# Kernel tuning notes

Hardware: AMD Instinct MI355X
Metric: run time of the kernel (lower is better)

## Reference

```python
import jax, jax.numpy as jnp
import numpy as np

PATCH = 16      # sqrt(n_patches=256)
ALPHA = 10.0
HEADS, DH = 2, 64


def _fourier(coords, Bm):
    # coords: (HW, 2), Bm: (n_features, 2) -> (HW, 2*n_features)
    proj = 2.0 * jnp.pi * coords @ Bm.T
    return jnp.concatenate([jnp.cos(proj), jnp.sin(proj)], axis=-1)


def _forward(coords_decoding, tokens, B_q, B_l0, B_l1,
             qW, qb, toqW, tokvW, tooW, toob,
             bwW0, bwb0, bwW1, bwb1,
             modW0, modb0, modW1, modb1,
             hvW0, hvb0, outW0, outb0, outW1, outb1):
    B = coords_decoding.shape[0]
    Hh, Ww = coords_decoding.shape[1], coords_decoding.shape[2]
    coords = coords_decoding.reshape(B, -1, coords_decoding.shape[-1])
    grid = coords[0]                      # (HW, 2); coords_modulation is None -> same grid
    HW = grid.shape[0]
    m = tokens.shape[1]

    # patch indices and spatial bias
    row = jnp.clip((grid[:, 0] * PATCH).astype(jnp.int32), 0, PATCH - 1)
    col = jnp.clip((grid[:, 1] * PATCH).astype(jnp.int32), 0, PATCH - 1)
    idx = row * PATCH + col               # (HW,)
    t = idx.astype(jnp.float32) / (PATCH * PATCH)
    pos = (jnp.arange(m, dtype=jnp.float32) + 0.5) / m
    rel = -ALPHA * jnp.abs(t[None, :] - pos[:, None]) ** 2   # (m, HW)
    bias = rel.T                          # (HW, m), broadcast over batch & heads

    # query features (shared across batch)
    xq = jax.nn.relu(_fourier(grid, B_q) @ qW + qb)           # (HW, hd)
    xq_b = jnp.broadcast_to(xq[None], (B, HW, xq.shape[-1]))

    # cross attention with spatial bias
    q = (xq_b @ toqW).reshape(B, HW, HEADS, DH).transpose(0, 2, 1, 3)   # (B,h,HW,Dh)
    kv = tokens @ tokvW                                                  # (B,m,2*inner)
    k, v = jnp.split(kv, 2, axis=-1)
    k = k.reshape(B, m, HEADS, DH).transpose(0, 2, 1, 3)                 # (B,h,m,Dh)
    v = v.reshape(B, m, HEADS, DH).transpose(0, 2, 1, 3)
    sim = jnp.einsum('bhqd,bhkd->bhqk', q, k) * (DH ** -0.5) + bias[None, None]
    attn = jax.nn.softmax(sim, axis=-1)
    o = jnp.einsum('bhqk,bhkd->bhqd', attn, v)
    o = o.transpose(0, 2, 1, 3).reshape(B, HW, HEADS * DH)
    mod = o @ tooW + toob                                                # (B,HW,hd)

    # per-band MLP stack (layer_num = 2)
    def band(Bl, bwW, bwb, mW, mb):
        h = jax.nn.relu(_fourier(grid, Bl) @ bwW + bwb)                  # (HW,hd)
        return jax.nn.relu(h[None] + mod @ mW + mb)                      # (B,HW,hd)

    m0 = band(B_l0, bwW0, bwb0, modW0, modb0)
    m1 = band(B_l1, bwW1, bwb1, modW1, modb1)
    hv0 = m0
    hv1 = jax.nn.relu((m1 + hv0) @ hvW0 + hvb0)
    out = (hv0 @ outW0 + outb0) + (hv1 @ outW1 + outb1)                  # (B,HW,3)
    return out.reshape(B, Hh, Ww, -1)


def setup_inputs() -> dict:
    key = jax.random.key(0)
    ks = jax.random.split(key, 32)
    B, H, W, L = 4, 128, 128, 256
    fd, hd, cd, od = 64, 256, 256, 3
    nf = fd // 2
    inner = HEADS * DH

    def lin(k, i, o):
        return jax.random.normal(k, (i, o), dtype=jnp.float32) / np.sqrt(i).astype(np.float32)

    inp = {}
    inp['coords_decoding'] = jax.random.uniform(ks[0], (B, H, W, 2), dtype=jnp.float32)
    inp['tokens'] = jax.random.normal(ks[1], (B, L, cd), dtype=jnp.float32)
    inp['B_q'] = jax.random.normal(ks[2], (nf, 2), dtype=jnp.float32) / 16.0
    inp['B_l0'] = jax.random.normal(ks[3], (nf, 2), dtype=jnp.float32) / 128.0
    inp['B_l1'] = jax.random.normal(ks[4], (nf, 2), dtype=jnp.float32) / 32.0
    inp['qW'] = lin(ks[5], fd, hd); inp['qb'] = jnp.zeros((hd,), jnp.float32)
    inp['toqW'] = lin(ks[6], hd, inner)
    inp['tokvW'] = lin(ks[7], cd, inner * 2)
    inp['tooW'] = lin(ks[8], inner, hd); inp['toob'] = jnp.zeros((hd,), jnp.float32)
    inp['bwW0'] = lin(ks[9], fd, hd); inp['bwb0'] = jnp.zeros((hd,), jnp.float32)
    inp['bwW1'] = lin(ks[10], fd, hd); inp['bwb1'] = jnp.zeros((hd,), jnp.float32)
    inp['modW0'] = lin(ks[11], hd, hd); inp['modb0'] = jnp.zeros((hd,), jnp.float32)
    inp['modW1'] = lin(ks[12], hd, hd); inp['modb1'] = jnp.zeros((hd,), jnp.float32)
    inp['hvW0'] = lin(ks[13], hd, hd); inp['hvb0'] = jnp.zeros((hd,), jnp.float32)
    inp['outW0'] = lin(ks[14], hd, od); inp['outb0'] = jnp.zeros((od,), jnp.float32)
    inp['outW1'] = lin(ks[15], hd, od); inp['outb1'] = jnp.zeros((od,), jnp.float32)
    return inp


def reference(coords_decoding, tokens, B_q, B_l0, B_l1,
              qW, qb, toqW, tokvW, tooW, toob,
              bwW0, bwb0, bwW1, bwb1,
              modW0, modb0, modW1, modb1,
              hvW0, hvb0, outW0, outb0, outW1, outb1):
    return _forward(coords_decoding, tokens, B_q, B_l0, B_l1,
                    qW, qb, toqW, tokvW, tooW, toob,
                    bwW0, bwb0, bwW1, bwb1,
                    modW0, modb0, modW1, modb1,
                    hvW0, hvb0, outW0, outb0, outW1, outb1)
```

## Files before the change

### kernel.cpp

```cpp
#include <hip/hip_runtime.h>
#include <stdint.h>

constexpr int kHW = 16384;
constexpr int kB  = 4;
constexpr int kM  = 256;

typedef _Float16 half8 __attribute__((ext_vector_type(8)));
typedef __attribute__((ext_vector_type(4))) float f32x4;

__device__ __forceinline__ unsigned short f2h(float f) {
  _Float16 h = (_Float16)f;
  return __builtin_bit_cast(unsigned short, h);
}
__device__ __forceinline__ float h2f(unsigned short u) {
  return (float)__builtin_bit_cast(_Float16, u);
}

__global__ __launch_bounds__(256) void wprep_kernel(
    const float* __restrict__ tooW, const float* __restrict__ modW0,
    const float* __restrict__ modW1, const float* __restrict__ hvW0,
    const float* __restrict__ qW, const float* __restrict__ bwW0,
    const float* __restrict__ bwW1, const float* __restrict__ toqW,
    unsigned short* __restrict__ tooWt, unsigned short* __restrict__ modW0t,
    unsigned short* __restrict__ modW1t, unsigned short* __restrict__ hvW0t,
    unsigned short* __restrict__ qWt, unsigned short* __restrict__ bw0t,
    unsigned short* __restrict__ bw1t, unsigned short* __restrict__ toqWt)
{
  int m = blockIdx.x, tid = threadIdx.x;
  const float* Ws[8] = {tooW, modW0, modW1, hvW0, qW, bwW0, bwW1, toqW};
  unsigned short* Wts[8] = {tooWt, modW0t, modW1t, hvW0t, qWt, bw0t, bw1t, toqWt};
  const int Ks[8] = {128, 256, 256, 256, 64, 64, 64, 256};
  const int Ns[8] = {256, 256, 256, 256, 256, 256, 256, 128};
  const float* W = Ws[m];
  unsigned short* Wt = Wts[m];
  int K = Ks[m], N = Ns[m];
  if (tid < N) {
    for (int kb = 0; kb < K / 8; kb++) {
      unsigned short sv[8];
#pragma unroll
      for (int i = 0; i < 8; i++)
        sv[i] = f2h(W[(kb * 8 + i) * N + tid]);
      *(uint4*)&Wt[tid * K + kb * 8] = *(const uint4*)sv;
    }
  }
}

__global__ __launch_bounds__(256) void kv_kernel(
    const float* __restrict__ tokens, const float* __restrict__ tokvW,
    unsigned short* __restrict__ kn_ws, unsigned short* __restrict__ vt_ws)
{
  __shared__ __align__(16) float tok[256];
  int b = blockIdx.y, j = blockIdx.x, c = threadIdx.x;
  tok[c] = tokens[(b * kM + j) * 256 + c];
  __syncthreads();
  float acc = 0.f;
  for (int i4 = 0; i4 < 64; i4++) {
    float4 t4 = *(const float4*)&tok[i4 * 4];
    acc += t4.x * tokvW[(i4*4+0)*256 + c] + t4.y * tokvW[(i4*4+1)*256 + c]
         + t4.z * tokvW[(i4*4+2)*256 + c] + t4.w * tokvW[(i4*4+3)*256 + c];
  }
  unsigned short hv = f2h(acc);
  if (c < 128) {
    int h = c >> 6, dd = c & 63;
    kn_ws[((size_t)(b*2+h)*256 + j) * 64 + dd] = hv;
  } else {
    int c2 = c - 128;
    int h = c2 >> 6, dd = c2 & 63;
    vt_ws[((size_t)(b*2+h)*64 + dd) * 256 + j] = hv;
  }
}

constexpr int kFPitch = 72;
constexpr int kXPitch = 264;

__global__ __launch_bounds__(256, 2) void feat_kernel(
    const float* __restrict__ coords,
    const float* __restrict__ Bq, const float* __restrict__ Bl0, const float* __restrict__ Bl1,
    const float* __restrict__ qb, const float* __restrict__ bwb0, const float* __restrict__ bwb1,
    const unsigned short* __restrict__ qWt, const unsigned short* __restrict__ bw0t,
    const unsigned short* __restrict__ bw1t, const unsigned short* __restrict__ toqWt,
    float* __restrict__ t_ws, unsigned short* __restrict__ qc_ws,
    unsigned short* __restrict__ h0_hf, unsigned short* __restrict__ h1_hf)
{
  __shared__ __align__(16) unsigned short ff_s[3][32][kFPitch];
  __shared__ __align__(16) unsigned short xq_s[32][kXPitch];
  __shared__ float coords_s[64];

  int tid = threadIdx.x;
  int px0 = blockIdx.x * 32;
  int w = tid >> 6, ln = tid & 63;
  int c = ln & 15, q = ln >> 4;

  if (tid < 64) coords_s[tid] = coords[px0 * 2 + tid];
  __syncthreads();

#pragma unroll
  for (int r = 0; r < 24; r++) {
    int v = r * 256 + tid;
    int mat = v >> 11;
    int p = (v >> 6) & 31;
    int f = v & 63;
    int fr = f & 31;
    const float* Bm = (mat == 0) ? Bq : (mat == 1 ? Bl0 : Bl1);
    float x = coords_s[p * 2 + 0];
    float y = coords_s[p * 2 + 1];
    float proj = 6.283185307179586f * (x * Bm[fr*2+0] + y * Bm[fr*2+1]);
    float s, cc;
    __sincosf(proj, &s, &cc);
    ff_s[mat][p][f] = f2h((f < 32) ? cc : s);
  }
  if (tid < 32) {
    float x = coords_s[tid * 2 + 0];
    float y = coords_s[tid * 2 + 1];
    int row = min(max((int)(x * 16.0f), 0), 15);
    int col = min(max((int)(y * 16.0f), 0), 15);
    t_ws[px0 + tid] = (float)(row * 16 + col) * (1.0f / 256.0f);
  }
  __syncthreads();

  const f32x4 zero4 = {0.f, 0.f, 0.f, 0.f};

  for (int mat = 0; mat < 3; mat++) {
    const unsigned short* Wt = (mat == 0) ? qWt : (mat == 1 ? bw0t : bw1t);
    const float* bias = (mat == 0) ? qb : (mat == 1 ? bwb0 : bwb1);
    f32x4 acc[8];
#pragma unroll
    for (int i = 0; i < 8; i++) acc[i] = zero4;
#pragma unroll
    for (int ks = 0; ks < 2; ks++) {
      int koff = ks * 32 + q * 8;
      half8 bfr[4];
#pragma unroll
      for (int nt = 0; nt < 4; nt++)
        bfr[nt] = *(const half8*)(Wt + (size_t)(w*64 + nt*16 + c) * 64 + koff);
      half8 afr[2];
#pragma unroll
      for (int mt = 0; mt < 2; mt++)
        afr[mt] = *(const half8*)(&ff_s[mat][mt*16 + c][koff]);
#pragma unroll
      for (int mt = 0; mt < 2; mt++)
#pragma unroll
        for (int nt = 0; nt < 4; nt++)
          acc[mt*4+nt] = __builtin_amdgcn_mfma_f32_16x16x32_f16(afr[mt], bfr[nt], acc[mt*4+nt], 0, 0, 0);
    }
    float bv[4];
#pragma unroll
    for (int nt = 0; nt < 4; nt++) bv[nt] = bias[w*64 + nt*16 + c];
#pragma unroll
    for (int mt = 0; mt < 2; mt++)
#pragma unroll
      for (int nt = 0; nt < 4; nt++)
#pragma unroll
        for (int rg = 0; rg < 4; rg++) {
          int row = mt*16 + q*4 + rg, col = w*64 + nt*16 + c;
          unsigned short hv = f2h(fmaxf(acc[mt*4+nt][rg] + bv[nt], 0.f));
          if (mat == 0)      xq_s[row][col] = hv;
          else if (mat == 1) h0_hf[((size_t)(px0 + row)) * 256 + col] = hv;
          else               h1_hf[((size_t)(px0 + row)) * 256 + col] = hv;
        }
  }
  __syncthreads();

  {
    f32x4 acc2[4];
#pragma unroll
    for (int i = 0; i < 4; i++) acc2[i] = zero4;
#pragma unroll
    for (int kt = 0; kt < 8; kt++) {
      int koff = kt * 32 + q * 8;
      half8 bfr[2];
#pragma unroll
      for (int nt = 0; nt < 2; nt++)
        bfr[nt] = *(const half8*)(toqWt + (size_t)(w*32 + nt*16 + c) * 256 + koff);
      half8 afr[2];
#pragma unroll
      for (int mt = 0; mt < 2; mt++)
        afr[mt] = *(const half8*)(&xq_s[mt*16 + c][koff]);
#pragma unroll
      for (int mt = 0; mt < 2; mt++)
#pragma unroll
        for (int nt = 0; nt < 2; nt++)
          acc2[mt*2+nt] = __builtin_amdgcn_mfma_f32_16x16x32_f16(afr[mt], bfr[nt], acc2[mt*2+nt], 0, 0, 0);
    }
#pragma unroll
    for (int mt = 0; mt < 2; mt++)
#pragma unroll
      for (int nt = 0; nt < 2; nt++)
#pragma unroll
        for (int rg = 0; rg < 4; rg++) {
          int row = mt*16 + q*4 + rg, col = w*32 + nt*16 + c;
          qc_ws[((size_t)(px0 + row)) * 128 + col] = f2h(acc2[mt*2+nt][rg]);
        }
  }
}

constexpr int kPPitch = 264;

__global__ __launch_bounds__(256, 2) void attn_kernel(
    const unsigned short* __restrict__ kn_ws,
    const unsigned short* __restrict__ vt_ws,
    const unsigned short* __restrict__ qc_ws,
    const float* __restrict__ t_ws,
    unsigned short* __restrict__ o_hf)
{
  __shared__ __align__(16) unsigned short P_s[32 * kPPitch];
  __shared__ float t_s[32];
  __shared__ float red_max[32][4];
  __shared__ float red_sum[32][4];

  int b = blockIdx.y;
  int px0 = blockIdx.x * 32;
  int tid = threadIdx.x;
  int w = tid >> 6, ln = tid & 63;
  int c = ln & 15, q = ln >> 4;

  if (tid < 32) t_s[tid] = t_ws[px0 + tid];

  const f32x4 zero4 = {0.f, 0.f, 0.f, 0.f};

  for (int h = 0; h < 2; h++) {
    __syncthreads();

    f32x4 acc[8];
#pragma unroll
    for (int i = 0; i < 8; i++) acc[i] = zero4;
    const unsigned short* kbase = kn_ws + (size_t)(b*2+h) * 256 * 64;
#pragma unroll
    for (int ks = 0; ks < 2; ks++) {
      int koff = ks * 32 + q * 8;
      half8 a0 = *(const half8*)(qc_ws + (size_t)(px0 + c) * 128 + h*64 + koff);
      half8 a1 = *(const half8*)(qc_ws + (size_t)(px0 + 16 + c) * 128 + h*64 + koff);
#pragma unroll
      for (int nt = 0; nt < 4; nt++) {
        half8 bf = *(const half8*)(kbase + (size_t)(w*64 + nt*16 + c) * 64 + koff);
        acc[0*4+nt] = __builtin_amdgcn_mfma_f32_16x16x32_f16(a0, bf, acc[0*4+nt], 0, 0, 0);
        acc[1*4+nt] = __builtin_amdgcn_mfma_f32_16x16x32_f16(a1, bf, acc[1*4+nt], 0, 0, 0);
      }
    }

    float lm[2][4];
#pragma unroll
    for (int mt = 0; mt < 2; mt++)
#pragma unroll
      for (int rg = 0; rg < 4; rg++) {
        int row = mt*16 + q*4 + rg;
        float tv = t_s[row];
        float mx = -1e30f;
#pragma unroll
        for (int nt = 0; nt < 4; nt++) {
          int token = w*64 + nt*16 + c;
          float pos = ((float)token + 0.5f) * (1.0f / 256.0f);
          float db = tv - pos;
          float sb = acc[mt*4+nt][rg] * 0.125f - 10.0f * db * db;
          acc[mt*4+nt][rg] = sb;
          mx = fmaxf(mx, sb);
        }
        lm[mt][rg] = mx;
      }
#pragma unroll
    for (int s = 1; s < 16; s <<= 1)
#pragma unroll
      for (int mt = 0; mt < 2; mt++)
#pragma unroll
        for (int rg = 0; rg < 4; rg++)
          lm[mt][rg] = fmaxf(lm[mt][rg], __shfl_xor(lm[mt][rg], s, 64));
    if (c == 0) {
#pragma unroll
      for (int mt = 0; mt < 2; mt++)
#pragma unroll
        for (int rg = 0; rg < 4; rg++)
          red_max[mt*16 + q*4 + rg][w] = lm[mt][rg];
    }
    __syncthreads();

    float ps[2][4];
#pragma unroll
    for (int mt = 0; mt < 2; mt++)
#pragma unroll
      for (int rg = 0; rg < 4; rg++) {
        int row = mt*16 + q*4 + rg;
        float gm = fmaxf(fmaxf(red_max[row][0], red_max[row][1]),
                         fmaxf(red_max[row][2], red_max[row][3]));
        float sum = 0.f;
#pragma unroll
        for (int nt = 0; nt < 4; nt++) {
          float e = __expf(acc[mt*4+nt][rg] - gm);
          sum += e;
          P_s[row * kPPitch + w*64 + nt*16 + c] = f2h(e);
        }
        ps[mt][rg] = sum;
      }
#pragma unroll
    for (int s = 1; s < 16; s <<= 1)
#pragma unroll
      for (int mt = 0; mt < 2; mt++)
#pragma unroll
        for (int rg = 0; rg < 4; rg++)
          ps[mt][rg] += __shfl_xor(ps[mt][rg], s, 64);
    if (c == 0) {
#pragma unroll
      for (int mt = 0; mt < 2; mt++)
#pragma unroll
        for (int rg = 0; rg < 4; rg++)
          red_sum[mt*16 + q*4 + rg][w] = ps[mt][rg];
    }
    __syncthreads();

    f32x4 oacc[2] = {zero4, zero4};
    const unsigned short* vbase = vt_ws + (size_t)(b*2+h) * 64 * 256;
#pragma unroll
    for (int kt = 0; kt < 8; kt++) {
      int koff = kt * 32 + q * 8;
      half8 bf = *(const half8*)(vbase + (size_t)(w*16 + c) * 256 + koff);
      half8 a0 = *(const half8*)(P_s + (0*16 + c) * kPPitch + koff);
      half8 a1 = *(const half8*)(P_s + (1*16 + c) * kPPitch + koff);
      oacc[0] = __builtin_amdgcn_mfma_f32_16x16x32_f16(a0, bf, oacc[0], 0, 0, 0);
      oacc[1] = __builtin_amdgcn_mfma_f32_16x16x32_f16(a1, bf, oacc[1], 0, 0, 0);
    }
#pragma unroll
    for (int mt = 0; mt < 2; mt++)
#pragma unroll
      for (int rg = 0; rg < 4; rg++) {
        int row = mt*16 + q*4 + rg;
        float rinv = 1.0f / (red_sum[row][0] + red_sum[row][1] +
                             red_sum[row][2] + red_sum[row][3]);
        o_hf[((size_t)(b * kHW + px0 + row)) * 128 + h*64 + w*16 + c] =
            f2h(oacc[mt][rg] * rinv);
      }
  }
}

constexpr int kPitch = 264;

template <int KD>
__device__ __forceinline__ void gemm4(
    const unsigned short* abuf, const unsigned short* wt,
    f32x4* acc , int c, int q)
{
#pragma unroll
  for (int ks = 0; ks < KD / 32; ks++) {
    int koff = ks * 32 + q * 8;
    half8 bfr[4];
#pragma unroll
    for (int nt = 0; nt < 4; nt++)
      bfr[nt] = *(const half8*)(wt + (nt * 16 + c) * KD + koff);
    half8 afr[4];
#pragma unroll
    for (int mt = 0; mt < 4; mt++)
      afr[mt] = *(const half8*)(abuf + (mt * 16 + c) * kPitch + koff);
#pragma unroll
    for (int mt = 0; mt < 4; mt++)
#pragma unroll
      for (int nt = 0; nt < 4; nt++)
        acc[mt * 4 + nt] = __builtin_amdgcn_mfma_f32_16x16x32_f16(afr[mt], bfr[nt], acc[mt * 4 + nt], 0, 0, 0);
  }
}

__global__ __launch_bounds__(256, 2) void mlp_kernel(
    const unsigned short* __restrict__ o_hf,
    const unsigned short* __restrict__ h0_hf, const unsigned short* __restrict__ h1_hf,
    const unsigned short* __restrict__ tooWt, const float* __restrict__ toob,
    const unsigned short* __restrict__ modW0t, const float* __restrict__ modb0,
    const unsigned short* __restrict__ modW1t, const float* __restrict__ modb1,
    const unsigned short* __restrict__ hvW0t, const float* __restrict__ hvb0,
    const float* __restrict__ outW0, const float* __restrict__ outb0,
    const float* __restrict__ outW1, const float* __restrict__ outb1,
    float* __restrict__ dout)
{
  __shared__ __align__(16) unsigned short buf0[64 * kPitch];
  __shared__ __align__(16) unsigned short buf1[64 * kPitch];
  __shared__ __align__(16) unsigned short hbuf[16 * kPitch];
  __shared__ __align__(16) float scratch[64 * 3 * 4];

  int tid = threadIdx.x;
  int px0 = blockIdx.x * 16;
  int w = tid >> 6, ln = tid & 63;
  int c = ln & 15, q = ln >> 4;

#pragma unroll
  for (int i = 0; i < 4; i++) {
    int idx = i * 256 + tid;
    int r = idx >> 4, c8 = (idx & 15) * 8;
    int b = r >> 4, px = r & 15;
    uint4 v = *(const uint4*)(o_hf + ((size_t)(b * kHW + px0 + px)) * 128 + c8);
    *(uint4*)&buf0[r * kPitch + c8] = v;
  }
#pragma unroll
  for (int i = 0; i < 2; i++) {
    int idx = i * 256 + tid;
    int p = idx >> 5, c8 = (idx & 31) * 8;
    uint4 v = *(const uint4*)(h0_hf + ((size_t)(px0 + p)) * 256 + c8);
    *(uint4*)&hbuf[p * kPitch + c8] = v;
  }
  __syncthreads();

  f32x4 acc[16];
  const f32x4 zero4 = {0.f, 0.f, 0.f, 0.f};

#pragma unroll
  for (int i = 0; i < 16; i++) acc[i] = zero4;
  gemm4<128>(buf0, tooWt + (size_t)w * 64 * 128, acc, c, q);
  {
    float bias[4];
#pragma unroll
    for (int nt = 0; nt < 4; nt++) bias[nt] = toob[w * 64 + nt * 16 + c];
#pragma unroll
    for (int mt = 0; mt < 4; mt++)
#pragma unroll
      for (int nt = 0; nt < 4; nt++)
#pragma unroll
        for (int rg = 0; rg < 4; rg++) {
          int row = mt * 16 + q * 4 + rg, col = w * 64 + nt * 16 + c;
          buf1[row * kPitch + col] = f2h(acc[mt * 4 + nt][rg] + bias[nt]);
        }
  }
  __syncthreads();

#pragma unroll
  for (int i = 0; i < 16; i++) acc[i] = zero4;
  gemm4<256>(buf1, modW0t + (size_t)w * 64 * 256, acc, c, q);
  {
    float bias[4], hr[4][4];
#pragma unroll
    for (int nt = 0; nt < 4; nt++) {
      int col = w * 64 + nt * 16 + c;
      bias[nt] = modb0[col];
#pragma unroll
      for (int rg = 0; rg < 4; rg++)
        hr[nt][rg] = h2f(hbuf[(q * 4 + rg) * kPitch + col]);
    }
#pragma unroll
    for (int mt = 0; mt < 4; mt++)
#pragma unroll
      for (int nt = 0; nt < 4; nt++)
#pragma unroll
        for (int rg = 0; rg < 4; rg++) {
          int row = mt * 16 + q * 4 + rg, col = w * 64 + nt * 16 + c;
          buf0[row * kPitch + col] =
              f2h(fmaxf(acc[mt * 4 + nt][rg] + bias[nt] + hr[nt][rg], 0.f));
        }
  }
  __syncthreads();

#pragma unroll
  for (int i = 0; i < 2; i++) {
    int idx = i * 256 + tid;
    int p = idx >> 5, c8 = (idx & 31) * 8;
    uint4 v = *(const uint4*)(h1_hf + ((size_t)(px0 + p)) * 256 + c8);
    *(uint4*)&hbuf[p * kPitch + c8] = v;
  }
#pragma unroll
  for (int i = 0; i < 16; i++) acc[i] = zero4;
  gemm4<256>(buf1, modW1t + (size_t)w * 64 * 256, acc, c, q);
  __syncthreads();
  {
    float bias[4], hr[4][4];
#pragma unroll
    for (int nt = 0; nt < 4; nt++) {
      int col = w * 64 + nt * 16 + c;
      bias[nt] = modb1[col];
#pragma unroll
      for (int rg = 0; rg < 4; rg++)
        hr[nt][rg] = h2f(hbuf[(q * 4 + rg) * kPitch + col]);
    }
#pragma unroll
    for (int mt = 0; mt < 4; mt++)
#pragma unroll
      for (int nt = 0; nt < 4; nt++)
#pragma unroll
        for (int rg = 0; rg < 4; rg++) {
          int row = mt * 16 + q * 4 + rg, col = w * 64 + nt * 16 + c;
          float m0v = h2f(buf0[row * kPitch + col]);
          float v = m0v + fmaxf(acc[mt * 4 + nt][rg] + bias[nt] + hr[nt][rg], 0.f);
          buf1[row * kPitch + col] = f2h(v);
        }
  }
  __syncthreads();

#pragma unroll
  for (int i = 0; i < 16; i++) acc[i] = zero4;
  gemm4<256>(buf1, hvW0t + (size_t)w * 64 * 256, acc, c, q);
  {
    float bias[4], w0v[4][3], w1v[4][3];
#pragma unroll
    for (int nt = 0; nt < 4; nt++) {
      int col = w * 64 + nt * 16 + c;
      bias[nt] = hvb0[col];
#pragma unroll
      for (int k = 0; k < 3; k++) {
        w0v[nt][k] = outW0[col * 3 + k];
        w1v[nt][k] = outW1[col * 3 + k];
      }
    }
#pragma unroll
    for (int mt = 0; mt < 4; mt++) {
      float pk[4][3];
#pragma unroll
      for (int rg = 0; rg < 4; rg++)
#pragma unroll
        for (int k = 0; k < 3; k++) pk[rg][k] = 0.f;
#pragma unroll
      for (int nt = 0; nt < 4; nt++) {
        int col = w * 64 + nt * 16 + c;
#pragma unroll
        for (int rg = 0; rg < 4; rg++) {
          int row = mt * 16 + q * 4 + rg;
          float hv1 = fmaxf(acc[mt * 4 + nt][rg] + bias[nt], 0.f);
          float m0v = h2f(buf0[row * kPitch + col]);
#pragma unroll
          for (int k = 0; k < 3; k++)
            pk[rg][k] += m0v * w0v[nt][k] + hv1 * w1v[nt][k];
        }
      }
#pragma unroll
      for (int s = 1; s < 16; s <<= 1)
#pragma unroll
        for (int rg = 0; rg < 4; rg++)
#pragma unroll
          for (int k = 0; k < 3; k++)
            pk[rg][k] += __shfl_xor(pk[rg][k], s, 64);
      if (c == 0) {
#pragma unroll
        for (int rg = 0; rg < 4; rg++) {
          int row = mt * 16 + q * 4 + rg;
#pragma unroll
          for (int k = 0; k < 3; k++)
            scratch[row * 12 + k * 4 + w] = pk[rg][k];
        }
      }
    }
  }
  __syncthreads();

  if (tid < 192) {
    int row = tid / 3, k = tid % 3;
    int b = row >> 4, px = px0 + (row & 15);
    float s = outb0[k] + outb1[k];
#pragma unroll
    for (int ww = 0; ww < 4; ww++) s += scratch[row * 12 + k * 4 + ww];
    dout[((size_t)b * kHW + px) * 3 + k] = s;
  }
}

extern "C" void kernel_launch(void* const* d_in, const int* in_sizes, int n_in,
                              void* d_out, int out_size, void* d_ws, size_t ws_size,
                              hipStream_t stream) {
  const float* coords = (const float*)d_in[0];
  const float* tokens = (const float*)d_in[1];
  const float* Bq     = (const float*)d_in[2];
  const float* Bl0    = (const float*)d_in[3];
  const float* Bl1    = (const float*)d_in[4];
  const float* qW     = (const float*)d_in[5];
  const float* qb     = (const float*)d_in[6];
  const float* toqW   = (const float*)d_in[7];
  const float* tokvW  = (const float*)d_in[8];
  const float* tooW   = (const float*)d_in[9];
  const float* toob   = (const float*)d_in[10];
  const float* bwW0   = (const float*)d_in[11];
  const float* bwb0   = (const float*)d_in[12];
  const float* bwW1   = (const float*)d_in[13];
  const float* bwb1   = (const float*)d_in[14];
  const float* modW0  = (const float*)d_in[15];
  const float* modb0  = (const float*)d_in[16];
  const float* modW1  = (const float*)d_in[17];
  const float* modb1  = (const float*)d_in[18];
  const float* hvW0   = (const float*)d_in[19];
  const float* hvb0   = (const float*)d_in[20];
  const float* outW0  = (const float*)d_in[21];
  const float* outb0  = (const float*)d_in[22];
  const float* outW1  = (const float*)d_in[23];
  const float* outb1  = (const float*)d_in[24];

  char* ws = (char*)d_ws;
  float*          t_ws   = (float*)(ws + 0);
  unsigned short* qc_ws  = (unsigned short*)(ws + 65536);
  unsigned short* h0_hf  = (unsigned short*)(ws + 4259840);
  unsigned short* h1_hf  = (unsigned short*)(ws + 12648448);
  unsigned short* o_hf   = (unsigned short*)(ws + 21037056);
  unsigned short* kn_ws  = (unsigned short*)(ws + 37814272);
  unsigned short* vt_ws  = (unsigned short*)(ws + 38076416);
  unsigned short* tooWt  = (unsigned short*)(ws + 38338560);
  unsigned short* modW0t = (unsigned short*)(ws + 38404096);
  unsigned short* modW1t = (unsigned short*)(ws + 38535168);
  unsigned short* hvW0t  = (unsigned short*)(ws + 38666240);
  unsigned short* qWt    = (unsigned short*)(ws + 38797312);
  unsigned short* bw0t   = (unsigned short*)(ws + 38830080);
  unsigned short* bw1t   = (unsigned short*)(ws + 38862848);
  unsigned short* toqWt  = (unsigned short*)(ws + 38895616);

  wprep_kernel<<<dim3(8), 256, 0, stream>>>(
      tooW, modW0, modW1, hvW0, qW, bwW0, bwW1, toqW,
      tooWt, modW0t, modW1t, hvW0t, qWt, bw0t, bw1t, toqWt);
  feat_kernel<<<dim3(kHW / 32), 256, 0, stream>>>(
      coords, Bq, Bl0, Bl1, qb, bwb0, bwb1,
      qWt, bw0t, bw1t, toqWt,
      t_ws, qc_ws, h0_hf, h1_hf);
  kv_kernel<<<dim3(kM, kB), 256, 0, stream>>>(tokens, tokvW, kn_ws, vt_ws);
  attn_kernel<<<dim3(kHW / 32, kB), 256, 0, stream>>>(kn_ws, vt_ws, qc_ws, t_ws, o_hf);
  mlp_kernel<<<dim3(kHW / 16), 256, 0, stream>>>(
      o_hf, h0_hf, h1_hf, tooWt, toob, modW0t, modb0, modW1t, modb1,
      hvW0t, hvb0, outW0, outb0, outW1, outb1, (float*)d_out);
}
```

Baseline: 257.3 us.

## Swizzle LDS buffers and keep m0 in registers to shrink MLP shared memory

Replaces the padded LDS pitches with XOR-swizzled layouts in both the attention P buffer and the MLP activation buffers. The MLP kernel now keeps the m0 activation packed as fp16 pairs in registers, so the second 64x256 LDS buffer is no longer needed. It also loads h0 and h1 together up front and raises the launch bound to three blocks per SM. The aim is to avoid bank conflicts and cut LDS use so more blocks fit per CU. The cost is 32 extra live registers per thread, which may cause spilling or work against the higher occupancy target.

Result: slower. 365.4 us (+42.0%).

```diff
diff --git a/kernel.cpp b/kernel.cpp
--- a/kernel.cpp
+++ b/kernel.cpp
@@ -14,6 +14,19 @@
 }
 __device__ __forceinline__ float h2f(unsigned short u) {
   return (float)__builtin_bit_cast(_Float16, u);
+}
+__device__ __forceinline__ float unpk(unsigned p, int hi) {
+  return h2f((unsigned short)(p >> (hi * 16)));
+}
+__device__ __forceinline__ int swz256(int row, int col) {
+  int ch = col >> 3;
+  ch = (ch & ~7) | ((ch ^ row) & 7);
+  return row * 256 + ch * 8 + (col & 7);
+}
+__device__ __forceinline__ int swz128(int row, int col) {
+  int ch = col >> 3;
+  ch = (ch & 8) | ((ch ^ row) & 7);
+  return row * 128 + ch * 8 + (col & 7);
 }
 
 __global__ __launch_bounds__(256) void wprep_kernel(
@@ -194,8 +207,6 @@
   }
 }
 
-constexpr int kPPitch = 264;
-
 __global__ __launch_bounds__(256, 2) void attn_kernel(
     const unsigned short* __restrict__ kn_ws,
     const unsigned short* __restrict__ vt_ws,
@@ -203,7 +214,7 @@
     const float* __restrict__ t_ws,
     unsigned short* __restrict__ o_hf)
 {
-  __shared__ __align__(16) unsigned short P_s[32 * kPPitch];
+  __shared__ __align__(16) unsigned short P_s[32 * 256];
   __shared__ float t_s[32];
   __shared__ float red_max[32][4];
   __shared__ float red_sum[32][4];
@@ -286,7 +297,7 @@
         for (int nt = 0; nt < 4; nt++) {
           float e = __expf(acc[mt*4+nt][rg] - gm);
           sum += e;
-          P_s[row * kPPitch + w*64 + nt*16 + c] = f2h(e);
+          P_s[swz256(row, w*64 + nt*16 + c)] = f2h(e);
         }
         ps[mt][rg] = sum;
       }
@@ -312,8 +323,8 @@
     for (int kt = 0; kt < 8; kt++) {
       int koff = kt * 32 + q * 8;
       half8 bf = *(const half8*)(vbase + (size_t)(w*16 + c) * 256 + koff);
-      half8 a0 = *(const half8*)(P_s + (0*16 + c) * kPPitch + koff);
-      half8 a1 = *(const half8*)(P_s + (1*16 + c) * kPPitch + koff);
+      half8 a0 = *(const half8*)(&P_s[swz256(c, koff)]);
+      half8 a1 = *(const half8*)(&P_s[swz256(16 + c, koff)]);
       oacc[0] = __builtin_amdgcn_mfma_f32_16x16x32_f16(a0, bf, oacc[0], 0, 0, 0);
       oacc[1] = __builtin_amdgcn_mfma_f32_16x16x32_f16(a1, bf, oacc[1], 0, 0, 0);
     }
@@ -330,33 +341,7 @@
   }
 }
 
-constexpr int kPitch = 264;
-
-template <int KD>
-__device__ __forceinline__ void gemm4(
-    const unsigned short* abuf, const unsigned short* wt,
-    f32x4* acc , int c, int q)
-{
-#pragma unroll
-  for (int ks = 0; ks < KD / 32; ks++) {
-    int koff = ks * 32 + q * 8;
-    half8 bfr[4];
-#pragma unroll
-    for (int nt = 0; nt < 4; nt++)
-      bfr[nt] = *(const half8*)(wt + (nt * 16 + c) * KD + koff);
-    half8 afr[4];
-#pragma unroll
-    for (int mt = 0; mt < 4; mt++)
-      afr[mt] = *(const half8*)(abuf + (mt * 16 + c) * kPitch + koff);
-#pragma unroll
-    for (int mt = 0; mt < 4; mt++)
-#pragma unroll
-      for (int nt = 0; nt < 4; nt++)
-        acc[mt * 4 + nt] = __builtin_amdgcn_mfma_f32_16x16x32_f16(afr[mt], bfr[nt], acc[mt * 4 + nt], 0, 0, 0);
-  }
-}
-
-__global__ __launch_bounds__(256, 2) void mlp_kernel(
+__global__ __launch_bounds__(256, 3) void mlp_kernel(
     const unsigned short* __restrict__ o_hf,
     const unsigned short* __restrict__ h0_hf, const unsigned short* __restrict__ h1_hf,
     const unsigned short* __restrict__ tooWt, const float* __restrict__ toob,
@@ -367,9 +352,8 @@
     const float* __restrict__ outW1, const float* __restrict__ outb1,
     float* __restrict__ dout)
 {
-  __shared__ __align__(16) unsigned short buf0[64 * kPitch];
-  __shared__ __align__(16) unsigned short buf1[64 * kPitch];
-  __shared__ __align__(16) unsigned short hbuf[16 * kPitch];
+  __shared__ __align__(16) unsigned short abuf[64 * 256];
+  __shared__ __align__(16) unsigned short obuf[8448];
   __shared__ __align__(16) float scratch[64 * 3 * 4];
 
   int tid = threadIdx.x;
@@ -377,109 +361,165 @@
   int w = tid >> 6, ln = tid & 63;
   int c = ln & 15, q = ln >> 4;
 
+  const f32x4 zero4 = {0.f, 0.f, 0.f, 0.f};
+  f32x4 acc[16];
+
 #pragma unroll
   for (int i = 0; i < 4; i++) {
     int idx = i * 256 + tid;
-    int r = idx >> 4, c8 = (idx & 15) * 8;
+    int r = idx >> 4, ch = idx & 15;
     int b = r >> 4, px = r & 15;
-    uint4 v = *(const uint4*)(o_hf + ((size_t)(b * kHW + px0 + px)) * 128 + c8);
-    *(uint4*)&buf0[r * kPitch + c8] = v;
+    uint4 v = *(const uint4*)(o_hf + ((size_t)(b * kHW + px0 + px)) * 128 + ch * 8);
+    *(uint4*)&obuf[swz128(r, ch * 8)] = v;
+  }
+  __syncthreads();
+
+#pragma unroll
+  for (int i = 0; i < 16; i++) acc[i] = zero4;
+#pragma unroll
+  for (int ks = 0; ks < 4; ks++) {
+    int koff = ks * 32 + q * 8;
+    half8 bfr[4];
+#pragma unroll
+    for (int nt = 0; nt < 4; nt++)
+      bfr[nt] = *(const half8*)(tooWt + (size_t)(w*64 + nt*16 + c) * 128 + koff);
+    half8 afr[4];
+#pragma unroll
+    for (int mt = 0; mt < 4; mt++)
+      afr[mt] = *(const half8*)&obuf[swz128(mt*16 + c, koff)];
+#pragma unroll
+    for (int mt = 0; mt < 4; mt++)
+#pragma unroll
+      for (int nt = 0; nt < 4; nt++)
+        acc[mt*4+nt] = __builtin_amdgcn_mfma_f32_16x16x32_f16(afr[mt], bfr[nt], acc[mt*4+nt], 0, 0, 0);
+  }
+  __syncthreads();
+
+  {
+    float bias[4];
+#pragma unroll
+    for (int nt = 0; nt < 4; nt++) bias[nt] = toob[w * 64 + nt * 16 + c];
+#pragma unroll
+    for (int mt = 0; mt < 4; mt++)
+#pragma unroll
+      for (int nt = 0; nt < 4; nt++)
+#pragma unroll
+        for (int rg = 0; rg < 4; rg++) {
+          int row = mt * 16 + q * 4 + rg, col = w * 64 + nt * 16 + c;
+          abuf[swz256(row, col)] = f2h(acc[mt * 4 + nt][rg] + bias[nt]);
+        }
   }
 #pragma unroll
   for (int i = 0; i < 2; i++) {
     int idx = i * 256 + tid;
     int p = idx >> 5, c8 = (idx & 31) * 8;
-    uint4 v = *(const uint4*)(h0_hf + ((size_t)(px0 + p)) * 256 + c8);
-    *(uint4*)&hbuf[p * kPitch + c8] = v;
-  }
-  __syncthreads();
-
-  f32x4 acc[16];
-  const f32x4 zero4 = {0.f, 0.f, 0.f, 0.f};
+    *(uint4*)&obuf[p * 264 + c8] =
+        *(const uint4*)(h0_hf + ((size_t)(px0 + p)) * 256 + c8);
+    *(uint4*)&obuf[4224 + p * 264 + c8] =
+        *(const uint4*)(h1_hf + ((size_t)(px0 + p)) * 256 + c8);
+  }
+  __syncthreads();
 
 #pragma unroll
   for (int i = 0; i < 16; i++) acc[i] = zero4;
-  gemm4<128>(buf0, tooWt + (size_t)w * 64 * 128, acc, c, q);
+#pragma unroll
+  for (int ks = 0; ks < 8; ks++) {
+    int koff = ks * 32 + q * 8;
+    half8 bfr[4];
+#pragma unroll
+    for (int nt = 0; nt < 4; nt++)
+      bfr[nt] = *(const half8*)(modW0t + (size_t)(w*64 + nt*16 + c) * 256 + koff);
+    half8 afr[4];
+#pragma unroll
+    for (int mt = 0; mt < 4; mt++)
+      afr[mt] = *(const half8*)&abuf[swz256(mt*16 + c, koff)];
+#pragma unroll
+    for (int mt = 0; mt < 4; mt++)
+#pragma unroll
+      for (int nt = 0; nt < 4; nt++)
+        acc[mt*4+nt] = __builtin_amdgcn_mfma_f32_16x16x32_f16(afr[mt], bfr[nt], acc[mt*4+nt], 0, 0, 0);
+  }
+  unsigned m0p[16][2];
   {
     float bias[4];
 #pragma unroll
-    for (int nt = 0; nt < 4; nt++) bias[nt] = toob[w * 64 + nt * 16 + c];
+    for (int nt = 0; nt < 4; nt++) bias[nt] = modb0[w * 64 + nt * 16 + c];
+#pragma unroll
+    for (int mt = 0; mt < 4; mt++)
+#pragma unroll
+      for (int nt = 0; nt < 4; nt++) {
+        int col = w * 64 + nt * 16 + c;
+        unsigned short hp[4];
+#pragma unroll
+        for (int rg = 0; rg < 4; rg++) {
+          float hv = h2f(obuf[(q * 4 + rg) * 264 + col]);
+          hp[rg] = f2h(fmaxf(acc[mt * 4 + nt][rg] + bias[nt] + hv, 0.f));
+        }
+        m0p[mt * 4 + nt][0] = (unsigned)hp[0] | ((unsigned)hp[1] << 16);
+        m0p[mt * 4 + nt][1] = (unsigned)hp[2] | ((unsigned)hp[3] << 16);
+      }
+  }
+
+#pragma unroll
+  for (int i = 0; i < 16; i++) acc[i] = zero4;
+#pragma unroll
+  for (int ks = 0; ks < 8; ks++) {
+    int koff = ks * 32 + q * 8;
+    half8 bfr[4];
+#pragma unroll
+    for (int nt = 0; nt < 4; nt++)
+      bfr[nt] = *(const half8*)(modW1t + (size_t)(w*64 + nt*16 + c) * 256 + koff);
+    half8 afr[4];
+#pragma unroll
+    for (int mt = 0; mt < 4; mt++)
+      afr[mt] = *(const half8*)&abuf[swz256(mt*16 + c, koff)];
 #pragma unroll
     for (int mt = 0; mt < 4; mt++)
 #pragma unroll
       for (int nt = 0; nt < 4; nt++)
+        acc[mt*4+nt] = __builtin_amdgcn_mfma_f32_16x16x32_f16(afr[mt], bfr[nt], acc[mt*4+nt], 0, 0, 0);
+  }
+  __syncthreads();
+  {
+    float bias[4];
+#pragma unroll
+    for (int nt = 0; nt < 4; nt++) bias[nt] = modb1[w * 64 + nt * 16 + c];
+#pragma unroll
+    for (int mt = 0; mt < 4; mt++)
+#pragma unroll
+      for (int nt = 0; nt < 4; nt++) {
+        int col = w * 64 + nt * 16 + c;
 #pragma unroll
         for (int rg = 0; rg < 4; rg++) {
-          int row = mt * 16 + q * 4 + rg, col = w * 64 + nt * 16 + c;
-          buf1[row * kPitch + col] = f2h(acc[mt * 4 + nt][rg] + bias[nt]);
-        }
+          int row = mt * 16 + q * 4 + rg;
+          float hv = h2f(obuf[4224 + (q * 4 + rg) * 264 + col]);
+          float m0v = unpk(m0p[mt * 4 + nt][rg >> 1], rg & 1);
+          float v = m0v + fmaxf(acc[mt * 4 + nt][rg] + bias[nt] + hv, 0.f);
+          abuf[swz256(row, col)] = f2h(v);
+        }
+      }
   }
   __syncthreads();
 
 #pragma unroll
   for (int i = 0; i < 16; i++) acc[i] = zero4;
-  gemm4<256>(buf1, modW0t + (size_t)w * 64 * 256, acc, c, q);
-  {
-    float bias[4], hr[4][4];
-#pragma unroll
-    for (int nt = 0; nt < 4; nt++) {
-      int col = w * 64 + nt * 16 + c;
-      bias[nt] = modb0[col];
-#pragma unroll
-      for (int rg = 0; rg < 4; rg++)
-        hr[nt][rg] = h2f(hbuf[(q * 4 + rg) * kPitch + col]);
-    }
+#pragma unroll
+  for (int ks = 0; ks < 8; ks++) {
+    int koff = ks * 32 + q * 8;
+    half8 bfr[4];
+#pragma unroll
+    for (int nt = 0; nt < 4; nt++)
+      bfr[nt] = *(const half8*)(hvW0t + (size_t)(w*64 + nt*16 + c) * 256 + koff);
+    half8 afr[4];
+#pragma unroll
+    for (int mt = 0; mt < 4; mt++)
+      afr[mt] = *(const half8*)&abuf[swz256(mt*16 + c, koff)];
 #pragma unroll
     for (int mt = 0; mt < 4; mt++)
 #pragma unroll
       for (int nt = 0; nt < 4; nt++)
-#pragma unroll
-        for (int rg = 0; rg < 4; rg++) {
-          int row = mt * 16 + q * 4 + rg, col = w * 64 + nt * 16 + c;
-          buf0[row * kPitch + col] =
-              f2h(fmaxf(acc[mt * 4 + nt][rg] + bias[nt] + hr[nt][rg], 0.f));
-        }
-  }
-  __syncthreads();
-
-#pragma unroll
-  for (int i = 0; i < 2; i++) {
-    int idx = i * 256 + tid;
-    int p = idx >> 5, c8 = (idx & 31) * 8;
-    uint4 v = *(const uint4*)(h1_hf + ((size_t)(px0 + p)) * 256 + c8);
-    *(uint4*)&hbuf[p * kPitch + c8] = v;
-  }
-#pragma unroll
-  for (int i = 0; i < 16; i++) acc[i] = zero4;
-  gemm4<256>(buf1, modW1t + (size_t)w * 64 * 256, acc, c, q);
-  __syncthreads();
-  {
-    float bias[4], hr[4][4];
-#pragma unroll
-    for (int nt = 0; nt < 4; nt++) {
-      int col = w * 64 + nt * 16 + c;
-      bias[nt] = modb1[col];
-#pragma unroll
-      for (int rg = 0; rg < 4; rg++)
-        hr[nt][rg] = h2f(hbuf[(q * 4 + rg) * kPitch + col]);
-    }
-#pragma unroll
-    for (int mt = 0; mt < 4; mt++)
-#pragma unroll
-      for (int nt = 0; nt < 4; nt++)
-#pragma unroll
-        for (int rg = 0; rg < 4; rg++) {
-          int row = mt * 16 + q * 4 + rg, col = w * 64 + nt * 16 + c;
-          float m0v = h2f(buf0[row * kPitch + col]);
-          float v = m0v + fmaxf(acc[mt * 4 + nt][rg] + bias[nt] + hr[nt][rg], 0.f);
-          buf1[row * kPitch + col] = f2h(v);
-        }
-  }
-  __syncthreads();
-
-#pragma unroll
-  for (int i = 0; i < 16; i++) acc[i] = zero4;
-  gemm4<256>(buf1, hvW0t + (size_t)w * 64 * 256, acc, c, q);
+        acc[mt*4+nt] = __builtin_amdgcn_mfma_f32_16x16x32_f16(afr[mt], bfr[nt], acc[mt*4+nt], 0, 0, 0);
+  }
   {
     float bias[4], w0v[4][3], w1v[4][3];
 #pragma unroll
@@ -501,12 +541,10 @@
         for (int k = 0; k < 3; k++) pk[rg][k] = 0.f;
 #pragma unroll
       for (int nt = 0; nt < 4; nt++) {
-        int col = w * 64 + nt * 16 + c;
 #pragma unroll
         for (int rg = 0; rg < 4; rg++) {
-          int row = mt * 16 + q * 4 + rg;
           float hv1 = fmaxf(acc[mt * 4 + nt][rg] + bias[nt], 0.f);
-          float m0v = h2f(buf0[row * kPitch + col]);
+          float m0v = unpk(m0p[mt * 4 + nt][rg >> 1], rg & 1);
 #pragma unroll
           for (int k = 0; k < 3; k++)
             pk[rg][k] += m0v * w0v[nt][k] + hv1 * w1v[nt][k];
```

## Give each attention wave full key rows to drop cross-wave softmax reductions

Applied to the files above, without the earlier changes.

The attention kernel now processes 64 pixels per block, with each wave owning 16 query rows and all 256 keys. Row max and sum therefore reduce within a wave by shuffles, which removes the shared-memory reduction arrays and two block barriers per head. The P tile is stored in an XOR-swizzled unpadded layout to avoid LDS bank conflicts, and the spatial bias index is computed inline from coords instead of being written by feat_kernel into a workspace. In exchange, each wave holds 16 accumulator tiles in registers, so register pressure and the risk of lower occupancy go up.

Measured after the change: 282.8 us. 1.1x slower.

```diff
diff --git a/kernel.cpp b/kernel.cpp
--- a/kernel.cpp
+++ b/kernel.cpp
@@ -14,6 +14,11 @@
 }
 __device__ __forceinline__ float h2f(unsigned short u) {
   return (float)__builtin_bit_cast(_Float16, u);
+}
+__device__ __forceinline__ int swz256(int row, int col) {
+  int ch = col >> 3;
+  ch = (ch & ~7) | ((ch ^ row) & 7);
+  return row * 256 + ch * 8 + (col & 7);
 }
 
 __global__ __launch_bounds__(256) void wprep_kernel(
@@ -79,7 +84,7 @@
     const float* __restrict__ qb, const float* __restrict__ bwb0, const float* __restrict__ bwb1,
     const unsigned short* __restrict__ qWt, const unsigned short* __restrict__ bw0t,
     const unsigned short* __restrict__ bw1t, const unsigned short* __restrict__ toqWt,
-    float* __restrict__ t_ws, unsigned short* __restrict__ qc_ws,
+    unsigned short* __restrict__ qc_ws,
     unsigned short* __restrict__ h0_hf, unsigned short* __restrict__ h1_hf)
 {
   __shared__ __align__(16) unsigned short ff_s[3][32][kFPitch];
@@ -109,13 +114,6 @@
     __sincosf(proj, &s, &cc);
     ff_s[mat][p][f] = f2h((f < 32) ? cc : s);
   }
-  if (tid < 32) {
-    float x = coords_s[tid * 2 + 0];
-    float y = coords_s[tid * 2 + 1];
-    int row = min(max((int)(x * 16.0f), 0), 15);
-    int col = min(max((int)(y * 16.0f), 0), 15);
-    t_ws[px0 + tid] = (float)(row * 16 + col) * (1.0f / 256.0f);
-  }
   __syncthreads();
 
   const f32x4 zero4 = {0.f, 0.f, 0.f, 0.f};
@@ -194,139 +192,116 @@
   }
 }
 
-constexpr int kPPitch = 264;
-
 __global__ __launch_bounds__(256, 2) void attn_kernel(
     const unsigned short* __restrict__ kn_ws,
     const unsigned short* __restrict__ vt_ws,
     const unsigned short* __restrict__ qc_ws,
-    const float* __restrict__ t_ws,
+    const float* __restrict__ coords,
     unsigned short* __restrict__ o_hf)
 {
-  __shared__ __align__(16) unsigned short P_s[32 * kPPitch];
-  __shared__ float t_s[32];
-  __shared__ float red_max[32][4];
-  __shared__ float red_sum[32][4];
+  __shared__ __align__(16) unsigned short P_s[64 * 256];
 
   int b = blockIdx.y;
-  int px0 = blockIdx.x * 32;
+  int px0 = blockIdx.x * 64;
   int tid = threadIdx.x;
   int w = tid >> 6, ln = tid & 63;
   int c = ln & 15, q = ln >> 4;
 
-  if (tid < 32) t_s[tid] = t_ws[px0 + tid];
+  float tv[4];
+#pragma unroll
+  for (int rg = 0; rg < 4; rg++) {
+    int px = px0 + w*16 + q*4 + rg;
+    float x = coords[px*2 + 0], y = coords[px*2 + 1];
+    int r = min(max((int)(x * 16.0f), 0), 15);
+    int cl = min(max((int)(y * 16.0f), 0), 15);
+    tv[rg] = (float)(r * 16 + cl) * (1.0f / 256.0f);
+  }
 
   const f32x4 zero4 = {0.f, 0.f, 0.f, 0.f};
 
   for (int h = 0; h < 2; h++) {
+    f32x4 acc[16];
+#pragma unroll
+    for (int i = 0; i < 16; i++) acc[i] = zero4;
+    const unsigned short* kbase = kn_ws + (size_t)(b*2+h) * 256 * 64;
+    const unsigned short* qrow = qc_ws + (size_t)(px0 + w*16 + c) * 128 + h*64;
+    half8 a0 = *(const half8*)(qrow + q*8);
+    half8 a1 = *(const half8*)(qrow + 32 + q*8);
+#pragma unroll
+    for (int nt = 0; nt < 16; nt++) {
+      const unsigned short* kr = kbase + (size_t)(nt*16 + c) * 64 + q*8;
+      half8 b0 = *(const half8*)(kr);
+      half8 b1 = *(const half8*)(kr + 32);
+      acc[nt] = __builtin_amdgcn_mfma_f32_16x16x32_f16(a0, b0, acc[nt], 0, 0, 0);
+      acc[nt] = __builtin_amdgcn_mfma_f32_16x16x32_f16(a1, b1, acc[nt], 0, 0, 0);
+    }
+
+    float lm[4];
+#pragma unroll
+    for (int rg = 0; rg < 4; rg++) {
+      float mx = -1e30f;
+#pragma unroll
+      for (int nt = 0; nt < 16; nt++) {
+        float pos = ((float)(nt*16 + c) + 0.5f) * (1.0f / 256.0f);
+        float db = tv[rg] - pos;
+        float sb = acc[nt][rg] * 0.125f - 10.0f * db * db;
+        acc[nt][rg] = sb;
+        mx = fmaxf(mx, sb);
+      }
+      lm[rg] = mx;
+    }
+#pragma unroll
+    for (int s = 1; s < 16; s <<= 1)
+#pragma unroll
+      for (int rg = 0; rg < 4; rg++)
+        lm[rg] = fmaxf(lm[rg], __shfl_xor(lm[rg], s, 64));
+
+    float linv[4];
+#pragma unroll
+    for (int rg = 0; rg < 4; rg++) {
+      float sum = 0.f;
+      int row = w*16 + q*4 + rg;
+#pragma unroll
+      for (int nt = 0; nt < 16; nt++) {
+        float e = __expf(acc[nt][rg] - lm[rg]);
+        sum += e;
+        P_s[swz256(row, nt*16 + c)] = f2h(e);
+      }
+      linv[rg] = sum;
+    }
+#pragma unroll
+    for (int s = 1; s < 16; s <<= 1)
+#pragma unroll
+      for (int rg = 0; rg < 4; rg++)
+        linv[rg] += __shfl_xor(linv[rg], s, 64);
+#pragma unroll
+    for (int rg = 0; rg < 4; rg++) linv[rg] = 1.0f / linv[rg];
+
     __syncthreads();
 
-    f32x4 acc[8];
-#pragma unroll
-    for (int i = 0; i < 8; i++) acc[i] = zero4;
-    const unsigned short* kbase = kn_ws + (size_t)(b*2+h) * 256 * 64;
-#pragma unroll
-    for (int ks = 0; ks < 2; ks++) {
-      int koff = ks * 32 + q * 8;
-      half8 a0 = *(const half8*)(qc_ws + (size_t)(px0 + c) * 128 + h*64 + koff);
-      half8 a1 = *(const half8*)(qc_ws + (size_t)(px0 + 16 + c) * 128 + h*64 + koff);
-#pragma unroll
-      for (int nt = 0; nt < 4; nt++) {
-        half8 bf = *(const half8*)(kbase + (size_t)(w*64 + nt*16 + c) * 64 + koff);
-        acc[0*4+nt] = __builtin_amdgcn_mfma_f32_16x16x32_f16(a0, bf, acc[0*4+nt], 0, 0, 0);
-        acc[1*4+nt] = __builtin_amdgcn_mfma_f32_16x16x32_f16(a1, bf, acc[1*4+nt], 0, 0, 0);
-      }
-    }
-
-    float lm[2][4];
-#pragma unroll
-    for (int mt = 0; mt < 2; mt++)
-#pragma unroll
-      for (int rg = 0; rg < 4; rg++) {
-        int row = mt*16 + q*4 + rg;
-        float tv = t_s[row];
-        float mx = -1e30f;
-#pragma unroll
-        for (int nt = 0; nt < 4; nt++) {
-          int token = w*64 + nt*16 + c;
-          float pos = ((float)token + 0.5f) * (1.0f / 256.0f);
-          float db = tv - pos;
-          float sb = acc[mt*4+nt][rg] * 0.125f - 10.0f * db * db;
-          acc[mt*4+nt][rg] = sb;
-          mx = fmaxf(mx, sb);
-        }
-        lm[mt][rg] = mx;
-      }
-#pragma unroll
-    for (int s = 1; s < 16; s <<= 1)
-#pragma unroll
-      for (int mt = 0; mt < 2; mt++)
-#pragma unroll
-        for (int rg = 0; rg < 4; rg++)
-          lm[mt][rg] = fmaxf(lm[mt][rg], __shfl_xor(lm[mt][rg], s, 64));
-    if (c == 0) {
-#pragma unroll
-      for (int mt = 0; mt < 2; mt++)
-#pragma unroll
-        for (int rg = 0; rg < 4; rg++)
-          red_max[mt*16 + q*4 + rg][w] = lm[mt][rg];
-    }
-    __syncthreads();
-
-    float ps[2][4];
-#pragma unroll
-    for (int mt = 0; mt < 2; mt++)
-#pragma unroll
-      for (int rg = 0; rg < 4; rg++) {
-        int row = mt*16 + q*4 + rg;
-        float gm = fmaxf(fmaxf(red_max[row][0], red_max[row][1]),
-                         fmaxf(red_max[row][2], red_max[row][3]));
-        float sum = 0.f;
-#pragma unroll
-        for (int nt = 0; nt < 4; nt++) {
-          float e = __expf(acc[mt*4+nt][rg] - gm);
-          sum += e;
-          P_s[row * kPPitch + w*64 + nt*16 + c] = f2h(e);
-        }
-        ps[mt][rg] = sum;
-      }
-#pragma unroll
-    for (int s = 1; s < 16; s <<= 1)
-#pragma unroll
-      for (int mt = 0; mt < 2; mt++)
-#pragma unroll
-        for (int rg = 0; rg < 4; rg++)
-          ps[mt][rg] += __shfl_xor(ps[mt][rg], s, 64);
-    if (c == 0) {
-#pragma unroll
-      for (int mt = 0; mt < 2; mt++)
-#pragma unroll
-        for (int rg = 0; rg < 4; rg++)
-          red_sum[mt*16 + q*4 + rg][w] = ps[mt][rg];
-    }
-    __syncthreads();
-
-    f32x4 oacc[2] = {zero4, zero4};
+    f32x4 oacc[4];
+#pragma unroll
+    for (int i = 0; i < 4; i++) oacc[i] = zero4;
     const unsigned short* vbase = vt_ws + (size_t)(b*2+h) * 64 * 256;
 #pragma unroll
     for (int kt = 0; kt < 8; kt++) {
       int koff = kt * 32 + q * 8;
-      half8 bf = *(const half8*)(vbase + (size_t)(w*16 + c) * 256 + koff);
-      half8 a0 = *(const half8*)(P_s + (0*16 + c) * kPPitch + koff);
-      half8 a1 = *(const half8*)(P_s + (1*16 + c) * kPPitch + koff);
-      oacc[0] = __builtin_amdgcn_mfma_f32_16x16x32_f16(a0, bf, oacc[0], 0, 0, 0);
-      oacc[1] = __builtin_amdgcn_mfma_f32_16x16x32_f16(a1, bf, oacc[1], 0, 0, 0);
-    }
-#pragma unroll
-    for (int mt = 0; mt < 2; mt++)
+      half8 af = *(const half8*)&P_s[swz256(w*16 + c, koff)];
+#pragma unroll
+      for (int nt = 0; nt < 4; nt++) {
+        half8 bf = *(const half8*)(vbase + (size_t)(nt*16 + c) * 256 + koff);
+        oacc[nt] = __builtin_amdgcn_mfma_f32_16x16x32_f16(af, bf, oacc[nt], 0, 0, 0);
+      }
+    }
+#pragma unroll
+    for (int nt = 0; nt < 4; nt++)
 #pragma unroll
       for (int rg = 0; rg < 4; rg++) {
-        int row = mt*16 + q*4 + rg;
-        float rinv = 1.0f / (red_sum[row][0] + red_sum[row][1] +
-                             red_sum[row][2] + red_sum[row][3]);
-        o_hf[((size_t)(b * kHW + px0 + row)) * 128 + h*64 + w*16 + c] =
-            f2h(oacc[mt][rg] * rinv);
-      }
+        int row = w*16 + q*4 + rg;
+        o_hf[((size_t)(b * kHW + px0 + row)) * 128 + h*64 + nt*16 + c] =
+            f2h(oacc[nt][rg] * linv[rg]);
+      }
+    __syncthreads();
   }
 }
 
@@ -572,7 +547,6 @@
   const float* outb1  = (const float*)d_in[24];
 
   char* ws = (char*)d_ws;
-  float*          t_ws   = (float*)(ws + 0);
   unsigned short* qc_ws  = (unsigned short*)(ws + 65536);
   unsigned short* h0_hf  = (unsigned short*)(ws + 4259840);
   unsigned short* h1_hf  = (unsigned short*)(ws + 12648448);
@@ -594,9 +568,9 @@
   feat_kernel<<<dim3(kHW / 32), 256, 0, stream>>>(
       coords, Bq, Bl0, Bl1, qb, bwb0, bwb1,
       qWt, bw0t, bw1t, toqWt,
-      t_ws, qc_ws, h0_hf, h1_hf);
+      qc_ws, h0_hf, h1_hf);
   kv_kernel<<<dim3(kM, kB), 256, 0, stream>>>(tokens, tokvW, kn_ws, vt_ws);
-  attn_kernel<<<dim3(kHW / 32, kB), 256, 0, stream>>>(kn_ws, vt_ws, qc_ws, t_ws, o_hf);
+  attn_kernel<<<dim3(kHW / 64, kB), 256, 0, stream>>>(kn_ws, vt_ws, qc_ws, coords, o_hf);
   mlp_kernel<<<dim3(kHW / 16), 256, 0, stream>>>(
       o_hf, h0_hf, h1_hf, tooWt, toob, modW0t, modb0, modW1t, modb1,
       hvW0t, hvb0, outW0, outb0, outW1, outb1, (float*)d_out);
```
